# Performance work log

Measured on AMD Instinct MI355X. Metric: run time of the kernel, lower is better.

## Reference

```python
import jax, jax.numpy as jnp
import numpy as np

NUM_NODES = 100000
NUM_EDGES = 640000
IN_DIM = 128
OUT_DIM = 128
NUM_REL = 16


def setup_inputs() -> dict:
    key = jax.random.key(0)
    k1, k2, k3, k4, k5 = jax.random.split(key, 5)
    x = jax.random.normal(k1, (NUM_NODES, IN_DIM), dtype=jnp.float32)
    edge_index = jax.random.randint(k2, (2, NUM_EDGES), 0, NUM_NODES, dtype=jnp.int64)
    edge_types = jax.random.randint(k3, (NUM_EDGES,), 0, NUM_REL, dtype=jnp.int64)
    # xavier-uniform-ish params
    rw_bound = float(np.sqrt(6.0 / (IN_DIM * OUT_DIM + NUM_REL)))
    relation_weights = jax.random.uniform(k4, (NUM_REL, IN_DIM, OUT_DIM), dtype=jnp.float32, minval=-rw_bound, maxval=rw_bound)
    sw_bound = float(np.sqrt(6.0 / (IN_DIM + OUT_DIM)))
    self_weight = jax.random.uniform(k5, (IN_DIM, OUT_DIM), dtype=jnp.float32, minval=-sw_bound, maxval=sw_bound)
    bias = jnp.zeros((OUT_DIM,), dtype=jnp.float32)
    return {
        'x': x,
        'edge_index': edge_index,
        'edge_types': edge_types,
        'relation_weights': relation_weights,
        'self_weight': self_weight,
        'bias': bias,
    }


def reference(x, edge_index, edge_types, relation_weights, self_weight, bias):
    num_nodes = x.shape[0]
    # self loop transform: (N, out)
    self_msg = x @ self_weight
    # transform all nodes by every relation weight once: (R, N, out)
    transformed = jnp.einsum('ni,rio->rno', x, relation_weights)
    src = edge_index[0]
    dst = edge_index[1]
    # per-edge message: pick (relation, source) transformed feature -> (E, out)
    msgs = transformed[edge_types, src]
    # scatter-add into destination nodes
    neighbor_msg = jax.ops.segment_sum(msgs, dst, num_segments=num_nodes)
    # dropout=0.0 (eval) -> identity
    return jax.nn.relu(self_msg + neighbor_msg + bias)
```

## Files before the change

kernel.cpp:

```cpp
#include <hip/hip_runtime.h>

#define N_NODES 100000
#define N_EDGES 640000
#define IN_DIM  128
#define OUT_DIM 128
#define N_REL   16
#define EPB     64
#define MEPB    128
#define SELF_PAD 100096
#define MAX_SLOTS (SELF_PAD + N_EDGES + 2048)
#define SENT    (N_EDGES + N_NODES)
#define MSG_ROWS (N_EDGES + N_NODES + 128)
#define NB_SCAN ((N_NODES + 255) / 256)
#define CVT_XB  (N_NODES * IN_DIM / 4 / 256)
#define CVT_WB  (17 * 16384 / 256)
#define HIST_B  ((N_EDGES + 255) / 256)
#define SELF_B  (SELF_PAD / 256)

typedef unsigned short u16;
typedef unsigned int   u32;
typedef __attribute__((ext_vector_type(8))) short bf16x8;
typedef __attribute__((ext_vector_type(4))) float f32x4;

__device__ inline u16 f2bf(float f) {
    u32 u = __builtin_bit_cast(u32, f);
    return (u16)((u + 0x7fffu + ((u >> 16) & 1u)) >> 16);
}
__device__ inline float bf2f(u16 s) {
    u32 u = ((u32)s) << 16;
    return __builtin_bit_cast(float, u);
}

__global__ __launch_bounds__(256) void k_pre(const float* __restrict__ x,
                                             const float* __restrict__ rw,
                                             const float* __restrict__ sw,
                                             const int* __restrict__ etype,
                                             const int* __restrict__ dst,
                                             u16* __restrict__ xb,
                                             u16* __restrict__ wt,
                                             int* __restrict__ counts_rel,
                                             int* __restrict__ dst_count,
                                             int* __restrict__ sorted) {
    int b = blockIdx.x, t = threadIdx.x;
    if (b < CVT_XB) {
        int i = b * 256 + t;
        float4 v = ((const float4*)x)[i];
        ushort4 p; p.x = f2bf(v.x); p.y = f2bf(v.y); p.z = f2bf(v.z); p.w = f2bf(v.w);
        ((ushort4*)xb)[i] = p;
    } else if (b < CVT_XB + CVT_WB) {
        int i = (b - CVT_XB) * 256 + t;
        int r = i >> 14, rem = i & 16383;
        int k = rem >> 7, np = rem & 127;
        float v = (r < 16) ? rw[i] : sw[rem];
        int c = np >> 4, nn = np & 15, kk = k >> 5, q = (k >> 3) & 3, j = k & 7;
        wt[(size_t)r * 16384 + (c * 4 + kk) * 512 + (q * 16 + nn) * 8 + j] = f2bf(v);
    } else if (b < CVT_XB + CVT_WB + HIST_B) {
        __shared__ int bins[N_REL];
        if (t < N_REL) bins[t] = 0;
        __syncthreads();
        int e = (b - CVT_XB - CVT_WB) * 256 + t;
        if (e < N_EDGES) {
            atomicAdd(&bins[etype[e]], 1);
            atomicAdd(&dst_count[dst[e]], 1);
        }
        __syncthreads();
        if (t < N_REL && bins[t]) atomicAdd(&counts_rel[t], bins[t]);
    } else {
        int i = (b - CVT_XB - CVT_WB - HIST_B) * 256 + t;
        sorted[i] = (i < N_NODES) ? (N_EDGES + i) : SENT;
    }
}

__global__ __launch_bounds__(256) void k_scan1(const int* __restrict__ dst_count,
                                               int* __restrict__ row_ptr,
                                               int* __restrict__ part) {
    __shared__ int buf[2][256];
    int t = threadIdx.x;
    int i = blockIdx.x * 256 + t;
    int v = (i < N_NODES) ? (dst_count[i] + 1) : 0;
    buf[0][t] = v;
    __syncthreads();
    int cur = 0;
    #pragma unroll
    for (int off = 1; off < 256; off <<= 1) {
        int nxt = cur ^ 1;
        int s = buf[cur][t];
        if (t >= off) s += buf[cur][t - off];
        buf[nxt][t] = s;
        __syncthreads();
        cur = nxt;
    }
    int inc = buf[cur][t];
    if (i < N_NODES) row_ptr[i] = inc - v;
    if (t == 255) part[blockIdx.x] = inc;
}

__global__ __launch_bounds__(512) void k_mid2(int* __restrict__ part,
                                              const int* __restrict__ counts,
                                              int* __restrict__ cursor,
                                              int* __restrict__ seg,
                                              int* __restrict__ sorted) {
    int t = threadIdx.x;
    if (blockIdx.x == 0) {
        __shared__ int buf[2][512];
        int v = (t < NB_SCAN) ? part[t] : 0;
        buf[0][t] = v;
        __syncthreads();
        int cur = 0;
        #pragma unroll
        for (int off = 1; off < 512; off <<= 1) {
            int nxt = cur ^ 1;
            int s = buf[cur][t];
            if (t >= off) s += buf[cur][t - off];
            buf[nxt][t] = s;
            __syncthreads();
            cur = nxt;
        }
        int inc = buf[cur][t];
        if (t < NB_SCAN) part[t] = inc - v;
    } else {
        __shared__ int s_seg[N_REL + 1];
        if (t == 0) {
            int s = SELF_PAD;
            for (int r = 0; r < N_REL; ++r) {
                cursor[r] = s; seg[r] = s; s_seg[r] = s;
                s += (counts[r] + 127) & ~127;
            }
            seg[N_REL] = s; s_seg[N_REL] = s;
        }
        __syncthreads();
        for (int r = 0; r < N_REL; ++r) {
            int b = s_seg[r] + counts[r], e2 = s_seg[r + 1];
            if (b + t < e2) sorted[b + t] = SENT;
        }
        for (int i = s_seg[N_REL] + t; i < MAX_SLOTS; i += 512)
            sorted[i] = SENT;
    }
}

__global__ __launch_bounds__(256) void k_scan3_scatter(int* __restrict__ row_ptr,
                                                       const int* __restrict__ part,
                                                       int* __restrict__ cursor_dst,
                                                       const int* __restrict__ etype,
                                                       int* __restrict__ cursor_rel,
                                                       int* __restrict__ sorted) {
    int t = threadIdx.x;
    if (blockIdx.x < NB_SCAN) {
        int i = blockIdx.x * 256 + t;
        if (i < N_NODES) {
            int r = row_ptr[i] + part[blockIdx.x];
            row_ptr[i] = r;
            cursor_dst[i] = r + 1;
        }
        if (i == 0) row_ptr[N_NODES] = N_EDGES + N_NODES;
    } else {
        __shared__ int bins[N_REL];
        __shared__ int base[N_REL];
        if (t < N_REL) bins[t] = 0;
        __syncthreads();
        int e = (blockIdx.x - NB_SCAN) * 256 + t;
        int rel = 0;
        bool valid = (e < N_EDGES);
        if (valid) { rel = etype[e]; atomicAdd(&bins[rel], 1); }
        __syncthreads();
        if (t < N_REL) {
            base[t] = bins[t] ? atomicAdd(&cursor_rel[t], bins[t]) : 0;
            bins[t] = 0;
        }
        __syncthreads();
        if (valid) {
            int p = atomicAdd(&bins[rel], 1);
            sorted[base[rel] + p] = e;
        }
    }
}

__global__ __launch_bounds__(256, 4) void k_msg_mfma(const u16* __restrict__ xb,
                                                     const u16* __restrict__ wt,
                                                     const int* __restrict__ src,
                                                     const int* __restrict__ etype,
                                                     const int* __restrict__ dst,
                                                     const int* __restrict__ sorted,
                                                     const int* __restrict__ row_ptr,
                                                     int* __restrict__ cursor_dst,
                                                     u16* __restrict__ msgs) {
    __shared__ u16 s_w[128 * 128];
    __shared__ int s_src[MEPB], s_pos[MEPB];
    int t = threadIdx.x;
    int e0 = blockIdx.x * MEPB;

    int ee0 = sorted[e0];
    int relb = (ee0 < N_EDGES) ? etype[ee0] : N_REL;
    const uint4* wsrc = (const uint4*)(wt + (size_t)relb * 16384);
    for (int i = t; i < 2048; i += 256)
        *(uint4*)&s_w[i * 8] = wsrc[i];
    if (t < MEPB) {
        int eid = sorted[e0 + t];
        int sv, pv;
        if (eid < N_EDGES) {
            sv = src[eid];
            pv = atomicAdd(&cursor_dst[dst[eid]], 1);
        } else if (eid < SENT) {
            sv = eid - N_EDGES;
            pv = row_ptr[sv];
        } else {
            sv = 0;
            pv = SENT + ((e0 + t) & 127);
        }
        s_src[t] = sv; s_pos[t] = pv;
    }
    __syncthreads();

    int wv = t >> 6, lane = t & 63;
    int n = lane & 15, q = lane >> 4;
    int eb = wv * 32;

    bf16x8 bx[2][4];
    int p[2];
    #pragma unroll
    for (int g = 0; g < 2; ++g) {
        int en = eb + g * 16 + n;
        const u16* xrow = xb + (size_t)s_src[en] * 128 + q * 8;
        p[g] = s_pos[en];
        #pragma unroll
        for (int kk = 0; kk < 4; ++kk)
            bx[g][kk] = *(const bf16x8*)(xrow + kk * 32);
    }

    uint4 uv[2][4];
    #pragma unroll
    for (int c = 0; c < 8; ++c) {
        bf16x8 aw[4];
        #pragma unroll
        for (int kk = 0; kk < 4; ++kk)
            aw[kk] = *(const bf16x8*)&s_w[(c * 4 + kk) * 512 + lane * 8];
        #pragma unroll
        for (int g = 0; g < 2; ++g) {
            f32x4 acc = {0.f, 0.f, 0.f, 0.f};
            #pragma unroll
            for (int kk = 0; kk < 4; ++kk)
                acc = __builtin_amdgcn_mfma_f32_16x16x32_bf16(aw[kk], bx[g][kk], acc, 0, 0, 0);
            u32 lo = (u32)f2bf(acc[0]) | ((u32)f2bf(acc[1]) << 16);
            u32 hi = (u32)f2bf(acc[2]) | ((u32)f2bf(acc[3]) << 16);
            if ((c & 1) == 0) { uv[g][c >> 1].x = lo; uv[g][c >> 1].y = hi; }
            else              { uv[g][c >> 1].z = lo; uv[g][c >> 1].w = hi; }
        }
    }
    #pragma unroll
    for (int g = 0; g < 2; ++g) {
        u32* mrow = (u32*)(msgs + (size_t)p[g] * 128 + q * 32);
        #pragma unroll
        for (int j = 0; j < 4; ++j)
            *(uint4*)(mrow + j * 4) = uv[g][j];
    }
}

__global__ __launch_bounds__(256) void k_gather(const int* __restrict__ row_ptr,
                                                const u16* __restrict__ msgs,
                                                const float* __restrict__ bias,
                                                float* __restrict__ out) {
    int wid  = (blockIdx.x * 256 + threadIdx.x) >> 6;
    int lane = threadIdx.x & 63;
    if (wid >= N_NODES) return;
    int r0 = row_ptr[wid], r1 = row_ptr[wid + 1];
    int h = lane & 15, quarter = lane >> 4;
    const uint4* m = (const uint4*)msgs;
    float s[8] = {0.f,0.f,0.f,0.f,0.f,0.f,0.f,0.f};
    int i = r0 + quarter;
    for (; i + 4 < r1; i += 8) {
        uint4 v = m[(size_t)i * 16 + h];
        uint4 w = m[(size_t)(i + 4) * 16 + h];
        s[0] += bf2f((u16)(v.x & 0xffffu)); s[1] += bf2f((u16)(v.x >> 16));
        s[2] += bf2f((u16)(v.y & 0xffffu)); s[3] += bf2f((u16)(v.y >> 16));
        s[4] += bf2f((u16)(v.z & 0xffffu)); s[5] += bf2f((u16)(v.z >> 16));
        s[6] += bf2f((u16)(v.w & 0xffffu)); s[7] += bf2f((u16)(v.w >> 16));
        s[0] += bf2f((u16)(w.x & 0xffffu)); s[1] += bf2f((u16)(w.x >> 16));
        s[2] += bf2f((u16)(w.y & 0xffffu)); s[3] += bf2f((u16)(w.y >> 16));
        s[4] += bf2f((u16)(w.z & 0xffffu)); s[5] += bf2f((u16)(w.z >> 16));
        s[6] += bf2f((u16)(w.w & 0xffffu)); s[7] += bf2f((u16)(w.w >> 16));
    }
    if (i < r1) {
        uint4 v = m[(size_t)i * 16 + h];
        s[0] += bf2f((u16)(v.x & 0xffffu)); s[1] += bf2f((u16)(v.x >> 16));
        s[2] += bf2f((u16)(v.y & 0xffffu)); s[3] += bf2f((u16)(v.y >> 16));
        s[4] += bf2f((u16)(v.z & 0xffffu)); s[5] += bf2f((u16)(v.z >> 16));
        s[6] += bf2f((u16)(v.w & 0xffffu)); s[7] += bf2f((u16)(v.w >> 16));
    }
    #pragma unroll
    for (int j = 0; j < 8; ++j) {
        s[j] += __shfl_xor(s[j], 16);
        s[j] += __shfl_xor(s[j], 32);
    }
    if (quarter == 0) {
        int c0 = (2 * h) & 7, c1 = (2 * h + 1) & 7, qq = h >> 2;
        float4 b0 = *(const float4*)&bias[c0 * 16 + qq * 4];
        float4 b1 = *(const float4*)&bias[c1 * 16 + qq * 4];
        float* ob = out + (size_t)wid * 128;
        float4 v0, v1;
        v0.x = fmaxf(s[0] + b0.x, 0.f); v0.y = fmaxf(s[1] + b0.y, 0.f);
        v0.z = fmaxf(s[2] + b0.z, 0.f); v0.w = fmaxf(s[3] + b0.w, 0.f);
        v1.x = fmaxf(s[4] + b1.x, 0.f); v1.y = fmaxf(s[5] + b1.y, 0.f);
        v1.z = fmaxf(s[6] + b1.z, 0.f); v1.w = fmaxf(s[7] + b1.w, 0.f);
        *(float4*)(ob + c0 * 16 + qq * 4) = v0;
        *(float4*)(ob + c1 * 16 + qq * 4) = v1;
    }
}

__global__ __launch_bounds__(128) void k_self_old(const float* __restrict__ x,
                                                  const float* __restrict__ sw,
                                                  const float* __restrict__ bias,
                                                  float* __restrict__ out) {
    __shared__ float s_x[8][IN_DIM];
    int t = threadIdx.x;
    int n0 = blockIdx.x * 8;
    for (int i = t; i < 8 * IN_DIM; i += 128) {
        int r = i >> 7, j = i & 127;
        s_x[r][j] = x[(size_t)(n0 + r) * IN_DIM + j];
    }
    __syncthreads();
    float acc[8] = {0.f,0.f,0.f,0.f,0.f,0.f,0.f,0.f};
    for (int k = 0; k < IN_DIM; ++k) {
        float w = sw[k * OUT_DIM + t];
        #pragma unroll
        for (int i = 0; i < 8; ++i) acc[i] += s_x[i][k] * w;
    }
    float b = bias[t];
    #pragma unroll
    for (int i = 0; i < 8; ++i)
        out[(size_t)(n0 + i) * OUT_DIM + t] = acc[i] + b;
}

__global__ __launch_bounds__(256) void k_hist_rel(const int* __restrict__ etype,
                                                  int* __restrict__ counts_rel) {
    __shared__ int bins[N_REL];
    int t = threadIdx.x;
    if (t < N_REL) bins[t] = 0;
    __syncthreads();
    int e = blockIdx.x * 256 + t;
    if (e < N_EDGES) atomicAdd(&bins[etype[e]], 1);
    __syncthreads();
    if (t < N_REL && bins[t]) atomicAdd(&counts_rel[t], bins[t]);
}

__global__ void k_scan_rel(const int* __restrict__ counts, int* __restrict__ cursor) {
    if (threadIdx.x == 0) {
        int s = 0;
        for (int r = 0; r < N_REL; ++r) { cursor[r] = s; s += counts[r]; }
    }
}

__global__ __launch_bounds__(256) void k_scatter_rel(const int* __restrict__ etype,
                                                     int* __restrict__ cursor,
                                                     int* __restrict__ sorted) {
    __shared__ int bins[N_REL];
    __shared__ int base[N_REL];
    int t = threadIdx.x;
    if (t < N_REL) bins[t] = 0;
    __syncthreads();
    int e = blockIdx.x * 256 + t;
    int rel = 0;
    bool valid = (e < N_EDGES);
    if (valid) { rel = etype[e]; atomicAdd(&bins[rel], 1); }
    __syncthreads();
    if (t < N_REL) {
        base[t] = bins[t] ? atomicAdd(&cursor[t], bins[t]) : 0;
        bins[t] = 0;
    }
    __syncthreads();
    if (valid) {
        int p = atomicAdd(&bins[rel], 1);
        sorted[base[rel] + p] = e;
    }
}

__global__ __launch_bounds__(256) void k_edge_atomic(const float* __restrict__ x,
                                              const float* __restrict__ rw,
                                              const int* __restrict__ src,
                                              const int* __restrict__ dst,
                                              const int* __restrict__ etype,
                                              const int* __restrict__ sorted,
                                              float* __restrict__ out) {
    __shared__ int s_src[EPB], s_dst[EPB], s_rel[EPB];
    __shared__ float s_x[EPB][IN_DIM];
    int t = threadIdx.x;
    int e0 = blockIdx.x * EPB;
    if (t < EPB) {
        int eid = sorted[e0 + t];
        s_src[t] = src[eid]; s_dst[t] = dst[eid]; s_rel[t] = etype[eid];
    }
    __syncthreads();
    for (int i = t; i < EPB * IN_DIM; i += 256) {
        int e = i >> 7, j = i & 127;
        s_x[e][j] = x[(size_t)s_src[e] * IN_DIM + j];
    }
    int rel0 = s_rel[0];
    bool uni = true;
    for (int i = 1; i < EPB; ++i) uni &= (s_rel[i] == rel0);
    __syncthreads();
    int cg = t & 31, eg = t >> 5;
    for (int i = 0; i < 8; ++i) {
        int e = eg * 8 + i;
        int rel = uni ? rel0 : s_rel[e];
        const float4* Wr = (const float4*)(rw + (size_t)rel * IN_DIM * OUT_DIM);
        float a0=0.f, a1=0.f, a2=0.f, a3=0.f;
        for (int k = 0; k < 128; ++k) {
            float4 w = Wr[k * 32 + cg];
            float xv = s_x[e][k];
            a0 += xv * w.x; a1 += xv * w.y; a2 += xv * w.z; a3 += xv * w.w;
        }
        float* o = out + (size_t)s_dst[e] * OUT_DIM + cg * 4;
        atomicAdd(o + 0, a0); atomicAdd(o + 1, a1);
        atomicAdd(o + 2, a2); atomicAdd(o + 3, a3);
    }
}

__global__ void k_relu(float* __restrict__ out) {
    int i = blockIdx.x * blockDim.x + threadIdx.x;
    float4* o4 = (float4*)out;
    const int n4 = N_NODES * OUT_DIM / 4;
    if (i < n4) {
        float4 v = o4[i];
        v.x = fmaxf(v.x, 0.f); v.y = fmaxf(v.y, 0.f);
        v.z = fmaxf(v.z, 0.f); v.w = fmaxf(v.w, 0.f);
        o4[i] = v;
    }
}

extern "C" void kernel_launch(void* const* d_in, const int* in_sizes, int n_in,
                              void* d_out, int out_size, void* d_ws, size_t ws_size,
                              hipStream_t stream) {
    const float* x     = (const float*)d_in[0];
    const int*   eidx  = (const int*)d_in[1];
    const int*   etype = (const int*)d_in[2];
    const float* rw    = (const float*)d_in[3];
    const float* sw    = (const float*)d_in[4];
    const float* bias  = (const float*)d_in[5];
    float* out = (float*)d_out;
    const int* src = eidx;
    const int* dst = eidx + N_EDGES;

    int* counts_rel = (int*)d_ws;
    int* cursor_rel = counts_rel + 16;
    int* seg        = cursor_rel + 16;
    int* part       = seg + 32;
    int* dst_count  = part + 512;
    int* row_ptr    = dst_count + N_NODES;
    int* cursor_dst = row_ptr + N_NODES + 1;
    int* sorted     = cursor_dst + N_NODES;
    size_t off = (((char*)(sorted + MAX_SLOTS) - (char*)d_ws) + 255) & ~(size_t)255;
    u16* xb   = (u16*)((char*)d_ws + off);
    u16* wtb  = xb + (size_t)N_NODES * 128;
    u16* msgs = wtb + 17 * 16384;
    size_t need = (size_t)((char*)(msgs + (size_t)MSG_ROWS * 128) - (char*)d_ws);

    const int MB = MAX_SLOTS / MEPB;

    if (ws_size >= need) {
        hipMemsetAsync(d_ws, 0, (size_t)(576 + N_NODES) * sizeof(int), stream);
        k_pre<<<CVT_XB + CVT_WB + HIST_B + SELF_B, 256, 0, stream>>>(
            x, rw, sw, etype, dst, xb, wtb, counts_rel, dst_count, sorted);
        k_scan1<<<NB_SCAN, 256, 0, stream>>>(dst_count, row_ptr, part);
        k_mid2<<<2, 512, 0, stream>>>(part, counts_rel, cursor_rel, seg, sorted);
        k_scan3_scatter<<<NB_SCAN + HIST_B, 256, 0, stream>>>(
            row_ptr, part, cursor_dst, etype, cursor_rel, sorted);

        k_msg_mfma<<<MB, 256, 0, stream>>>(xb, wtb, src, etype, dst, sorted,
                                           row_ptr, cursor_dst, msgs);
        k_gather<<<(N_NODES * 64 + 255) / 256, 256, 0, stream>>>(row_ptr, msgs, bias, out);
    } else {
        hipMemsetAsync(counts_rel, 0, 16 * sizeof(int), stream);
        k_hist_rel<<<HIST_B, 256, 0, stream>>>(etype, counts_rel);
        k_scan_rel<<<1, 64, 0, stream>>>(counts_rel, cursor_rel);
        k_scatter_rel<<<HIST_B, 256, 0, stream>>>(etype, cursor_rel, sorted);
        k_self_old<<<N_NODES / 8, 128, 0, stream>>>(x, sw, bias, out);
        k_edge_atomic<<<N_EDGES / EPB, 256, 0, stream>>>(x, rw, src, dst, etype, sorted, out);
        k_relu<<<(N_NODES * OUT_DIM / 4 + 255) / 256, 256, 0, stream>>>(out);
    }
}
```

Before: 321.5 us.

## Sort edges by source-node bucket and relation to improve gather locality

Edges are now grouped into runs keyed by (source bucket of 2048 nodes, relation), with self-loop rows placed in a per-bucket 17th run, instead of being sorted by relation alone. Each message block then reads source rows from a narrow node range, so the bf16 x gathers are meant to hit cache better. The relation and self-loop segments become a 833-entry scan done by a 1024-thread block. Padding each run to 128 adds many sentinel slots, and fully empty blocks exit early. In exchange, global atomics on the run counters replace the shared-memory histograms.

After: 580.1 us. 1.8x slower.

```diff
diff --git a/kernel.cpp b/kernel.cpp
--- a/kernel.cpp
+++ b/kernel.cpp
@@ -7,15 +7,18 @@
 #define N_REL   16
 #define EPB     64
 #define MEPB    128
-#define SELF_PAD 100096
-#define MAX_SLOTS (SELF_PAD + N_EDGES + 2048)
 #define SENT    (N_EDGES + N_NODES)
 #define MSG_ROWS (N_EDGES + N_NODES + 128)
 #define NB_SCAN ((N_NODES + 255) / 256)
 #define CVT_XB  (N_NODES * IN_DIM / 4 / 256)
 #define CVT_WB  (17 * 16384 / 256)
 #define HIST_B  ((N_EDGES + 255) / 256)
-#define SELF_B  (SELF_PAD / 256)
+#define BSH     11
+#define NBUK    49
+#define NRUN    (NBUK * 17)
+#define MAX_SLOTS 845824
+#define SFB     (MAX_SLOTS / 256)
+#define MB      (MAX_SLOTS / MEPB)
 
 typedef unsigned short u16;
 typedef unsigned int   u32;
@@ -34,11 +37,12 @@
 __global__ __launch_bounds__(256) void k_pre(const float* __restrict__ x,
                                              const float* __restrict__ rw,
                                              const float* __restrict__ sw,
+                                             const int* __restrict__ src,
                                              const int* __restrict__ etype,
                                              const int* __restrict__ dst,
                                              u16* __restrict__ xb,
                                              u16* __restrict__ wt,
-                                             int* __restrict__ counts_rel,
+                                             int* __restrict__ counts_run,
                                              int* __restrict__ dst_count,
                                              int* __restrict__ sorted) {
     int b = blockIdx.x, t = threadIdx.x;
@@ -55,19 +59,14 @@
         int c = np >> 4, nn = np & 15, kk = k >> 5, q = (k >> 3) & 3, j = k & 7;
         wt[(size_t)r * 16384 + (c * 4 + kk) * 512 + (q * 16 + nn) * 8 + j] = f2bf(v);
     } else if (b < CVT_XB + CVT_WB + HIST_B) {
-        __shared__ int bins[N_REL];
-        if (t < N_REL) bins[t] = 0;
-        __syncthreads();
         int e = (b - CVT_XB - CVT_WB) * 256 + t;
         if (e < N_EDGES) {
-            atomicAdd(&bins[etype[e]], 1);
+            atomicAdd(&counts_run[(src[e] >> BSH) * 17 + etype[e]], 1);
             atomicAdd(&dst_count[dst[e]], 1);
         }
-        __syncthreads();
-        if (t < N_REL && bins[t]) atomicAdd(&counts_rel[t], bins[t]);
     } else {
         int i = (b - CVT_XB - CVT_WB - HIST_B) * 256 + t;
-        sorted[i] = (i < N_NODES) ? (N_EDGES + i) : SENT;
+        sorted[i] = SENT;
     }
 }
 
@@ -95,20 +94,19 @@
     if (t == 255) part[blockIdx.x] = inc;
 }
 
-__global__ __launch_bounds__(512) void k_mid2(int* __restrict__ part,
-                                              const int* __restrict__ counts,
-                                              int* __restrict__ cursor,
-                                              int* __restrict__ seg,
-                                              int* __restrict__ sorted) {
+__global__ __launch_bounds__(1024) void k_mid2(int* __restrict__ part,
+                                               const int* __restrict__ counts_run,
+                                               int* __restrict__ cursor_run,
+                                               int* __restrict__ seg) {
+    __shared__ int buf[2][1024];
     int t = threadIdx.x;
     if (blockIdx.x == 0) {
-        __shared__ int buf[2][512];
         int v = (t < NB_SCAN) ? part[t] : 0;
         buf[0][t] = v;
         __syncthreads();
         int cur = 0;
         #pragma unroll
-        for (int off = 1; off < 512; off <<= 1) {
+        for (int off = 1; off < 1024; off <<= 1) {
             int nxt = cur ^ 1;
             int s = buf[cur][t];
             if (t >= off) s += buf[cur][t - off];
@@ -119,30 +117,38 @@
         int inc = buf[cur][t];
         if (t < NB_SCAN) part[t] = inc - v;
     } else {
-        __shared__ int s_seg[N_REL + 1];
-        if (t == 0) {
-            int s = SELF_PAD;
-            for (int r = 0; r < N_REL; ++r) {
-                cursor[r] = s; seg[r] = s; s_seg[r] = s;
-                s += (counts[r] + 127) & ~127;
-            }
-            seg[N_REL] = s; s_seg[N_REL] = s;
-        }
+        int cnt = 0;
+        if (t < NRUN) {
+            cnt = counts_run[t];
+            if (t % 17 == 16)
+                cnt += min(2048, N_NODES - ((t / 17) << BSH));
+            cnt = (cnt + 127) & ~127;
+        }
+        buf[0][t] = cnt;
         __syncthreads();
-        for (int r = 0; r < N_REL; ++r) {
-            int b = s_seg[r] + counts[r], e2 = s_seg[r + 1];
-            if (b + t < e2) sorted[b + t] = SENT;
-        }
-        for (int i = s_seg[N_REL] + t; i < MAX_SLOTS; i += 512)
-            sorted[i] = SENT;
+        int cur = 0;
+        #pragma unroll
+        for (int off = 1; off < 1024; off <<= 1) {
+            int nxt = cur ^ 1;
+            int s = buf[cur][t];
+            if (t >= off) s += buf[cur][t - off];
+            buf[nxt][t] = s;
+            __syncthreads();
+            cur = nxt;
+        }
+        int inc = buf[cur][t];
+        if (t < NRUN) { cursor_run[t] = inc - cnt; seg[t] = inc - cnt; }
+        if (t == NRUN - 1) seg[NRUN] = inc;
     }
 }
 
 __global__ __launch_bounds__(256) void k_scan3_scatter(int* __restrict__ row_ptr,
                                                        const int* __restrict__ part,
                                                        int* __restrict__ cursor_dst,
+                                                       const int* __restrict__ src,
                                                        const int* __restrict__ etype,
-                                                       int* __restrict__ cursor_rel,
+                                                       const int* __restrict__ seg,
+                                                       int* __restrict__ cursor_run,
                                                        int* __restrict__ sorted) {
     int t = threadIdx.x;
     if (blockIdx.x < NB_SCAN) {
@@ -151,26 +157,15 @@
             int r = row_ptr[i] + part[blockIdx.x];
             row_ptr[i] = r;
             cursor_dst[i] = r + 1;
+            sorted[seg[(i >> BSH) * 17 + 16] + (i & 2047)] = N_EDGES + i;
         }
         if (i == 0) row_ptr[N_NODES] = N_EDGES + N_NODES;
     } else {
-        __shared__ int bins[N_REL];
-        __shared__ int base[N_REL];
-        if (t < N_REL) bins[t] = 0;
-        __syncthreads();
         int e = (blockIdx.x - NB_SCAN) * 256 + t;
-        int rel = 0;
-        bool valid = (e < N_EDGES);
-        if (valid) { rel = etype[e]; atomicAdd(&bins[rel], 1); }
-        __syncthreads();
-        if (t < N_REL) {
-            base[t] = bins[t] ? atomicAdd(&cursor_rel[t], bins[t]) : 0;
-            bins[t] = 0;
-        }
-        __syncthreads();
-        if (valid) {
-            int p = atomicAdd(&bins[rel], 1);
-            sorted[base[rel] + p] = e;
+        if (e < N_EDGES) {
+            int run = (src[e] >> BSH) * 17 + etype[e];
+            int p = atomicAdd(&cursor_run[run], 1);
+            sorted[p] = e;
         }
     }
 }
@@ -190,6 +185,7 @@
     int e0 = blockIdx.x * MEPB;
 
     int ee0 = sorted[e0];
+    if (ee0 >= SENT) return;
     int relb = (ee0 < N_EDGES) ? etype[ee0] : N_REL;
     const uint4* wsrc = (const uint4*)(wt + (size_t)relb * 16384);
     for (int i = t; i < 2048; i += 256)
@@ -439,10 +435,10 @@
     const int* src = eidx;
     const int* dst = eidx + N_EDGES;
 
-    int* counts_rel = (int*)d_ws;
-    int* cursor_rel = counts_rel + 16;
-    int* seg        = cursor_rel + 16;
-    int* part       = seg + 32;
+    int* counts_run = (int*)d_ws;
+    int* cursor_run = counts_run + 1024;
+    int* seg        = cursor_run + 1024;
+    int* part       = seg + 1024;
     int* dst_count  = part + 512;
     int* row_ptr    = dst_count + N_NODES;
     int* cursor_dst = row_ptr + N_NODES + 1;
@@ -453,27 +449,28 @@
     u16* msgs = wtb + 17 * 16384;
     size_t need = (size_t)((char*)(msgs + (size_t)MSG_ROWS * 128) - (char*)d_ws);
 
-    const int MB = MAX_SLOTS / MEPB;
-
     if (ws_size >= need) {
-        hipMemsetAsync(d_ws, 0, (size_t)(576 + N_NODES) * sizeof(int), stream);
-        k_pre<<<CVT_XB + CVT_WB + HIST_B + SELF_B, 256, 0, stream>>>(
-            x, rw, sw, etype, dst, xb, wtb, counts_rel, dst_count, sorted);
+        hipMemsetAsync(d_ws, 0, (size_t)(1024 * 3 + 512 + N_NODES) * sizeof(int), stream);
+        k_pre<<<CVT_XB + CVT_WB + HIST_B + SFB, 256, 0, stream>>>(
+            x, rw, sw, src, etype, dst, xb, wtb, counts_run, dst_count, sorted);
         k_scan1<<<NB_SCAN, 256, 0, stream>>>(dst_count, row_ptr, part);
-        k_mid2<<<2, 512, 0, stream>>>(part, counts_rel, cursor_rel, seg, sorted);
+        k_mid2<<<2, 1024, 0, stream>>>(part, counts_run, cursor_run, seg);
         k_scan3_scatter<<<NB_SCAN + HIST_B, 256, 0, stream>>>(
-            row_ptr, part, cursor_dst, etype, cursor_rel, sorted);
+            row_ptr, part, cursor_dst, src, etype, seg, cursor_run, sorted);
 
         k_msg_mfma<<<MB, 256, 0, stream>>>(xb, wtb, src, etype, dst, sorted,
                                            row_ptr, cursor_dst, msgs);
         k_gather<<<(N_NODES * 64 + 255) / 256, 256, 0, stream>>>(row_ptr, msgs, bias, out);
     } else {
+        int* counts_rel = (int*)d_ws;
+        int* cursor_rel = counts_rel + 16;
+        int* sortedf    = counts_rel + 64;
         hipMemsetAsync(counts_rel, 0, 16 * sizeof(int), stream);
         k_hist_rel<<<HIST_B, 256, 0, stream>>>(etype, counts_rel);
         k_scan_rel<<<1, 64, 0, stream>>>(counts_rel, cursor_rel);
-        k_scatter_rel<<<HIST_B, 256, 0, stream>>>(etype, cursor_rel, sorted);
+        k_scatter_rel<<<HIST_B, 256, 0, stream>>>(etype, cursor_rel, sortedf);
         k_self_old<<<N_NODES / 8, 128, 0, stream>>>(x, sw, bias, out);
-        k_edge_atomic<<<N_EDGES / EPB, 256, 0, stream>>>(x, rw, src, dst, etype, sorted, out);
+        k_edge_atomic<<<N_EDGES / EPB, 256, 0, stream>>>(x, rw, src, dst, etype, sortedf, out);
         k_relu<<<(N_NODES * OUT_DIM / 4 + 255) / 256, 256, 0, stream>>>(out);
     }
 }
```

## Remap message blocks per XCD, early-exit padding blocks, issue gathers before weight staging

Applied to the files above, without the earlier changes.

The message kernel now remaps block indices so each XCD processes a contiguous range of sorted edges, meaning blocks that share a relation weight sit on the same L2. Blocks whose first slot is a padding sentinel exit immediately. Each wave now loads its source indices straight from global memory and starts the x-row gathers before staging the weights in LDS, so that gather latency overlaps the LDS fill and the atomics. The trade-off is that sorted is read twice and the remap arithmetic assumes blocks are dispatched round-robin across 8 XCDs.

After: 332.1 us. 1.03x slower.

```diff
diff --git a/kernel.cpp b/kernel.cpp
--- a/kernel.cpp
+++ b/kernel.cpp
@@ -16,6 +16,7 @@
 #define CVT_WB  (17 * 16384 / 256)
 #define HIST_B  ((N_EDGES + 255) / 256)
 #define SELF_B  (SELF_PAD / 256)
+#define MB      (MAX_SLOTS / MEPB)
 
 typedef unsigned short u16;
 typedef unsigned int   u32;
@@ -185,47 +186,46 @@
                                                      int* __restrict__ cursor_dst,
                                                      u16* __restrict__ msgs) {
     __shared__ u16 s_w[128 * 128];
-    __shared__ int s_src[MEPB], s_pos[MEPB];
-    int t = threadIdx.x;
-    int e0 = blockIdx.x * MEPB;
+    __shared__ int s_pos[MEPB];
+    int t = threadIdx.x;
+    const int q8 = MB >> 3, r8 = MB & 7;
+    int xcd = blockIdx.x & 7, idx = blockIdx.x >> 3;
+    int bid = (xcd < r8 ? xcd * (q8 + 1) : r8 * (q8 + 1) + (xcd - r8) * q8) + idx;
+    int e0 = bid * MEPB;
 
     int ee0 = sorted[e0];
+    if (ee0 >= SENT) return;
     int relb = (ee0 < N_EDGES) ? etype[ee0] : N_REL;
+
+    int wv = t >> 6, lane = t & 63;
+    int n = lane & 15, q = lane >> 4;
+    int eb = wv * 32;
+
+    bf16x8 bx[2][4];
+    #pragma unroll
+    for (int g = 0; g < 2; ++g) {
+        int eid = sorted[e0 + eb + g * 16 + n];
+        int sv = (eid < N_EDGES) ? src[eid]
+               : (eid < SENT)    ? eid - N_EDGES : 0;
+        const u16* xrow = xb + (size_t)sv * 128 + q * 8;
+        #pragma unroll
+        for (int kk = 0; kk < 4; ++kk)
+            bx[g][kk] = *(const bf16x8*)(xrow + kk * 32);
+    }
+
     const uint4* wsrc = (const uint4*)(wt + (size_t)relb * 16384);
     for (int i = t; i < 2048; i += 256)
         *(uint4*)&s_w[i * 8] = wsrc[i];
+
     if (t < MEPB) {
         int eid = sorted[e0 + t];
-        int sv, pv;
-        if (eid < N_EDGES) {
-            sv = src[eid];
-            pv = atomicAdd(&cursor_dst[dst[eid]], 1);
-        } else if (eid < SENT) {
-            sv = eid - N_EDGES;
-            pv = row_ptr[sv];
-        } else {
-            sv = 0;
-            pv = SENT + ((e0 + t) & 127);
-        }
-        s_src[t] = sv; s_pos[t] = pv;
-    }
-    __syncthreads();
-
-    int wv = t >> 6, lane = t & 63;
-    int n = lane & 15, q = lane >> 4;
-    int eb = wv * 32;
-
-    bf16x8 bx[2][4];
-    int p[2];
-    #pragma unroll
-    for (int g = 0; g < 2; ++g) {
-        int en = eb + g * 16 + n;
-        const u16* xrow = xb + (size_t)s_src[en] * 128 + q * 8;
-        p[g] = s_pos[en];
-        #pragma unroll
-        for (int kk = 0; kk < 4; ++kk)
-            bx[g][kk] = *(const bf16x8*)(xrow + kk * 32);
-    }
+        int pv;
+        if (eid < N_EDGES)   pv = atomicAdd(&cursor_dst[dst[eid]], 1);
+        else if (eid < SENT) pv = row_ptr[eid - N_EDGES];
+        else                 pv = SENT + ((e0 + t) & 127);
+        s_pos[t] = pv;
+    }
+    __syncthreads();
 
     uint4 uv[2][4];
     #pragma unroll
@@ -248,7 +248,8 @@
     }
     #pragma unroll
     for (int g = 0; g < 2; ++g) {
-        u32* mrow = (u32*)(msgs + (size_t)p[g] * 128 + q * 32);
+        int p = s_pos[eb + g * 16 + n];
+        u32* mrow = (u32*)(msgs + (size_t)p * 128 + q * 32);
         #pragma unroll
         for (int j = 0; j < 4; ++j)
             *(uint4*)(mrow + j * 4) = uv[g][j];
@@ -453,8 +454,6 @@
     u16* msgs = wtb + 17 * 16384;
     size_t need = (size_t)((char*)(msgs + (size_t)MSG_ROWS * 128) - (char*)d_ws);
 
-    const int MB = MAX_SLOTS / MEPB;
-
     if (ws_size >= need) {
         hipMemsetAsync(d_ws, 0, (size_t)(576 + N_NODES) * sizeof(int), stream);
         k_pre<<<CVT_XB + CVT_WB + HIST_B + SELF_B, 256, 0, stream>>>(
```
